# Kernel tuning notes

Measured on AMD Instinct MI355X. Metric: run time of the kernel, lower is better.

## Reference

```python
import jax, jax.numpy as jnp
import numpy as np

N_GRAPHS = 1000
P = 300                 # nodes per ring graph
N = N_GRAPHS * P        # 300000 nodes
IN_DIM = 2
HID = 128
OUT_DIM = 2


def _ring_edges():
    idx = jnp.arange(N)
    g = idx // P
    pos = idx % P
    nxt = g * P + (pos + 1) % P
    src = jnp.concatenate([idx, nxt])
    dst = jnp.concatenate([nxt, idx])
    return jnp.stack([src, dst]), g


def setup_inputs() -> dict:
    key = jax.random.key(0)
    ks = jax.random.split(key, 11)
    edge_index, batch = _ring_edges()
    x = jax.random.normal(ks[0], (N, IN_DIM), jnp.float32)

    def glorot(k, fan_in, fan_out):
        lim = np.sqrt(6.0 / (fan_in + fan_out)).astype(np.float32)
        return jax.random.uniform(k, (fan_in, fan_out), jnp.float32, -lim, lim)

    return {
        "x": x,
        "edge_index": edge_index,
        "batch": batch,
        "W1": glorot(ks[1], IN_DIM, HID), "b1": jnp.zeros((HID,), jnp.float32),
        "W2": glorot(ks[2], HID, HID),    "b2": jnp.zeros((HID,), jnp.float32),
        "W3": glorot(ks[3], HID, HID),    "b3": jnp.zeros((HID,), jnp.float32),
        "fw1": glorot(ks[4], HID, HID),   "fb1": jnp.zeros((HID,), jnp.float32),
        "fw2": glorot(ks[5], HID, OUT_DIM), "fb2": jnp.zeros((OUT_DIM,), jnp.float32),
    }


def _gcn_conv(x, W, b, src, dst, norm):
    h = x @ W                              # [N, out]
    msg = h[src] * norm[:, None]           # gather + per-edge scale
    agg = jax.ops.segment_sum(msg, dst, num_segments=N)  # scatter-add
    return agg + b


def reference(x, edge_index, batch, W1, b1, W2, b2, W3, b3, fw1, fb1, fw2, fb2):
    loop = jnp.arange(N)
    src = jnp.concatenate([edge_index[0], loop])
    dst = jnp.concatenate([edge_index[1], loop])
    deg = jax.ops.segment_sum(jnp.ones_like(dst, jnp.float32), dst, num_segments=N)
    dis = jax.lax.rsqrt(deg)               # deg >= 1 due to self-loops
    norm = dis[src] * dis[dst]             # per-edge normalization

    h = jax.nn.relu(_gcn_conv(x, W1, b1, src, dst, norm))
    h = jax.nn.relu(_gcn_conv(h, W2, b2, src, dst, norm))
    h = jax.nn.relu(_gcn_conv(h, W3, b3, src, dst, norm))

    # global mean pool per graph
    sums = jax.ops.segment_sum(h, batch, num_segments=N_GRAPHS)
    cnts = jax.ops.segment_sum(jnp.ones((N,), jnp.float32), batch, num_segments=N_GRAPHS)
    pooled = sums / cnts[:, None]

    out = jax.nn.relu(pooled @ fw1 + fb1)
    out = out @ fw2 + fb2
    return out
```

## Files before the change

### kernel.cpp

```cpp
#include <hip/hip_runtime.h>
#include <hip/hip_bf16.h>
#include <stdint.h>

#define P    300
#define HID  128
#define NG   1000
#define NTL  19

typedef __attribute__((ext_vector_type(8))) short bf16x8;
typedef __attribute__((ext_vector_type(4))) short bf16x4;
typedef __attribute__((ext_vector_type(4))) float f32x4;

__device__ short g_wsw[2 * HID * HID];

__device__ __forceinline__ short f2bf(float f) {
    union { float f; uint32_t u; } v; v.f = f;
    uint32_t r = v.u + 0x7fffu + ((v.u >> 16) & 1u);
    return (short)(r >> 16);
}
__device__ __forceinline__ uint32_t pkbf2(float a, float b) {
    union { __hip_bfloat162 h; uint32_t u; } cv;
    cv.h = __float22bfloat162_rn(float2{a, b});
    return cv.u;
}

__device__ __forceinline__ f32x4 mfma16(bf16x4 a, bf16x4 b, f32x4 c) {
#if __has_builtin(__builtin_amdgcn_mfma_f32_16x16x16bf16_1k)
    return __builtin_amdgcn_mfma_f32_16x16x16bf16_1k(a, b, c, 0, 0, 0);
#else
    asm("v_mfma_f32_16x16x16_bf16 %0, %1, %2, %0" : "+v"(c) : "v"(a), "v"(b));
    return c;
#endif
}

__global__ __launch_bounds__(256) void k_prep(const float* __restrict__ W2,
                                              const float* __restrict__ W3) {
    int b = blockIdx.x;
    const bool perm = (b < 8);
    const float* W = perm ? W2 : W3;
    short* dst = g_wsw + (perm ? 0 : HID * HID);
    int t    = (b & 7) * 256 + threadIdx.x;
    int fkey = t >> 4;
    int kc   = t & 15;
    int fsrc;
    if (perm) {
        int u = fkey >> 5, ft = (fkey >> 4) & 1, l = fkey & 15;
        fsrc = u * 32 + 2 * l + ft;
    } else fsrc = fkey;
    bf16x8 o;
    #pragma unroll
    for (int j = 0; j < 8; ++j)
        o[j] = f2bf(W[(kc * 8 + j) * HID + fsrc]);
    *(bf16x8*)&dst[(fkey * 16 + (kc ^ (fkey & 15))) * 8] = o;
}

template<int POOL>
__device__ __forceinline__ void run_pass(short* __restrict__ buf,
                                         const short* __restrict__ wbase,
                                         const float* __restrict__ bias,
                                         float* __restrict__ pool, int tid) {
    const int lane = tid & 63, wv = tid >> 6, q = lane >> 4, lm = lane & 15;
    const int ftg0 = wv * 2;
    bf16x8 wf[2][4];
    #pragma unroll
    for (int ft = 0; ft < 2; ++ft) {
        int fkey = (ftg0 + ft) * 16 + lm;
        #pragma unroll
        for (int kk = 0; kk < 4; ++kk)
            wf[ft][kk] = *(const bf16x8*)&wbase[(fkey * 16 + ((4 * kk + q) ^ lm)) * 8];
    }
    float biaf[2];
    #pragma unroll
    for (int ft = 0; ft < 2; ++ft)
        biaf[ft] = POOL ? bias[(ftg0 + ft) * 16 + lm] : bias[wv * 32 + 2 * lm + ft];
    const int fpair = wv * 32 + 2 * lm;
    const int kcs = fpair >> 3, offs = fpair & 7;

    const short ONE = (short)0x3F80;
    bf16x4 Sb = {0, 0, 0, 0}, Sp = {0, 0, 0, 0}, Sn = {0, 0, 0, 0},
           Swa = {0, 0, 0, 0}, Swb = {0, 0, 0, 0};
    #pragma unroll
    for (int j = 0; j < 4; ++j) {
        const int k = 4 * q + j;
        if (((lm & 3) == 0 && k == lm - 1) || ((lm & 3) == 3 && k == lm + 1))
            Sb[j] = ONE;
        if (lm == 0  && k == 15) Sp[j]  = ONE;
        if (lm == 15 && k == 0 ) Sn[j]  = ONE;
        if (lm == 11 && k == 0 ) Swa[j] = ONE;
        if (lm == 0  && k == 11) Swb[j] = ONE;
    }

    float psum[2] = {0.f, 0.f};

    auto mfma_tile = [&](int t, f32x4 (&G)[2]) {
        const short* tb = buf + t * 2048;
        G[0] = f32x4{0.f, 0.f, 0.f, 0.f};
        G[1] = f32x4{0.f, 0.f, 0.f, 0.f};
        #pragma unroll
        for (int kk = 0; kk < 4; ++kk) {
            bf16x8 af = *(const bf16x8*)&tb[(lm * 16 + ((4 * kk + q) ^ lm)) * 8];
            G[0] = __builtin_amdgcn_mfma_f32_16x16x32_bf16(af, wf[0][kk], G[0], 0, 0, 0);
            G[1] = __builtin_amdgcn_mfma_f32_16x16x32_bf16(af, wf[1][kk], G[1], 0, 0, 0);
        }
    };
    auto pack = [&](const f32x4 (&G)[2], bf16x4 (&d)[2]) {
        #pragma unroll
        for (int ft = 0; ft < 2; ++ft) {
            union { bf16x4 v; uint32_t u[2]; } pk;
            pk.u[0] = pkbf2(G[ft][0], G[ft][1]);
            pk.u[1] = pkbf2(G[ft][2], G[ft][3]);
            d[ft] = pk.v;
        }
    };
    auto store_rows = [&](int T, float (&o)[2][4]) {
        #pragma unroll
        for (int i = 0; i < 4; ++i) {
            int node = T * 16 + q * 4 + i;
            *(uint32_t*)&buf[(node * 16 + (kcs ^ (node & 15))) * 8 + offs] =
                pkbf2(o[0][i], o[1][i]);
        }
    };
    auto accum = [&](float (&o)[2][4]) {
        #pragma unroll
        for (int ft = 0; ft < 2; ++ft)
            psum[ft] += o[ft][0] + o[ft][1] + o[ft][2] + o[ft][3];
    };

    auto epi = [&](const f32x4 (&E)[2], const bf16x4 (&bT)[2],
                   const bf16x4 (&bP)[2], const bf16x4 (&bN)[2],
                   int wrap, const bf16x4 (&bW)[2], float (&o)[2][4]) {
        #pragma unroll
        for (int ft = 0; ft < 2; ++ft) {
            f32x4 C = {0.f, 0.f, 0.f, 0.f};
            C = mfma16(Sb, bT[ft], C);
            C = mfma16(Sp, bP[ft], C);
            C = mfma16(Sn, bN[ft], C);
            if (wrap == 1) C = mfma16(Swa, bW[ft], C);
            if (wrap == 2) C = mfma16(Swb, bW[ft], C);
            const float s0 = E[ft][0] + E[ft][1];
            const float s2 = E[ft][2] + E[ft][3];
            float t0 = C[0] + s0;
            float t1 = s0 + E[ft][2];
            float t2 = E[ft][1] + s2;
            float t3 = s2 + C[3];
            float v0 = fmaf(t0, 1.f / 3.f, biaf[ft]);
            float v1 = fmaf(t1, 1.f / 3.f, biaf[ft]);
            float v2 = fmaf(t2, 1.f / 3.f, biaf[ft]);
            float v3 = fmaf(t3, 1.f / 3.f, biaf[ft]);
            o[ft][0] = v0 > 0.f ? v0 : 0.f;
            o[ft][1] = v1 > 0.f ? v1 : 0.f;
            o[ft][2] = v2 > 0.f ? v2 : 0.f;
            o[ft][3] = v3 > 0.f ? v3 : 0.f;
        }
    };

    f32x4 G0c[2], Gp[2], Ga[2], Gb[2];
    bf16x4 bq0[2], bq1[2], bqA[2], bqB[2], bqC[2], bqD[2];

    mfma_tile(0, G0c);
    pack(G0c, bq0);
    bqB[0] = bq0[0]; bqB[1] = bq0[1];
    bqA[0] = bq0[0]; bqA[1] = bq0[1];
    Gp[0] = G0c[0]; Gp[1] = G0c[1];

    for (int j = 1; j <= 9; ++j) {
        mfma_tile(2 * j - 1, Ga); pack(Ga, bqC);
        mfma_tile(2 * j,     Gb); pack(Gb, bqD);
        if (j == 1) { bq1[0] = bqC[0]; bq1[1] = bqC[1]; }
        if (!POOL) __syncthreads();
        if (j > 1) {
            float o[2][4];
            epi(Gp, bqB, bqA, bqC, 0, bq0, o);
            if (POOL) accum(o); else store_rows(2 * j - 2, o);
        }
        {
            float o[2][4];
            epi(Ga, bqC, bqB, bqD, 0, bq0, o);
            if (POOL) accum(o); else store_rows(2 * j - 1, o);
        }
        Gp[0] = Gb[0]; Gp[1] = Gb[1];
        bqA[0] = bqC[0]; bqA[1] = bqC[1];
        bqB[0] = bqD[0]; bqB[1] = bqD[1];
    }

    {
        float o18[2][4];
        epi(Gp, bqB, bqA, bq0, 1, bq0, o18);
        if (q < 3) { if (POOL) accum(o18); else store_rows(18, o18); }
        float o0[2][4];
        epi(G0c, bq0, bqB, bq1, 2, bqB, o0);
        if (POOL) accum(o0); else store_rows(0, o0);
    }

    if (POOL) {
        #pragma unroll
        for (int ft = 0; ft < 2; ++ft) {
            psum[ft] += __shfl_xor(psum[ft], 16, 64);
            psum[ft] += __shfl_xor(psum[ft], 32, 64);
        }
        if (q == 0) {
            pool[ftg0 * 16 + lm]      = psum[0];
            pool[ftg0 * 16 + 16 + lm] = psum[1];
        }
    }
}

__global__ __launch_bounds__(256, 1) void k_graph(
        const float* __restrict__ x,
        const float* __restrict__ W1,  const float* __restrict__ b1,
        const float* __restrict__ b2v, const float* __restrict__ b3v,
        const float* __restrict__ fw1, const float* __restrict__ fb1,
        const float* __restrict__ fw2, const float* __restrict__ fb2,
        float* __restrict__ out) {
    __shared__ __align__(16) short buf[304 * HID];
    __shared__ __align__(16) float scr[640];
    float* xs    = scr;
    float* pool  = scr;
    float* parts = scr + 128;
    float* s1    = scr + 384;

    const int g = blockIdx.x, tid = threadIdx.x;

    if (tid < 150) *(float4*)&xs[tid * 4] = *(const float4*)&x[g * 600 + tid * 4];
    __syncthreads();

    {
        const int kc1 = tid & 15;
        const int n0  = tid >> 4;
        float w1x[8], w1y[8], b1v[8];
        #pragma unroll
        for (int j = 0; j < 8; ++j) {
            w1x[j] = W1[kc1 * 8 + j];
            w1y[j] = W1[HID + kc1 * 8 + j];
            b1v[j] = b1[kc1 * 8 + j];
        }
        #pragma unroll
        for (int it = 0; it < NTL; ++it) {
            int node = it * 16 + n0;
            uint32_t w[4] = {0u, 0u, 0u, 0u};
            if (node < P) {
                int prev = (node == 0)     ? P - 1 : node - 1;
                int next = (node == P - 1) ? 0     : node + 1;
                float2 xp = *(const float2*)&xs[2 * prev];
                float2 xc = *(const float2*)&xs[2 * node];
                float2 xn = *(const float2*)&xs[2 * next];
                float ax = (xp.x + xc.x + xn.x) * (1.f / 3.f);
                float ay = (xp.y + xc.y + xn.y) * (1.f / 3.f);
                #pragma unroll
                for (int jj = 0; jj < 4; ++jj) {
                    float va = ax * w1x[2*jj]   + ay * w1y[2*jj]   + b1v[2*jj];
                    float vb = ax * w1x[2*jj+1] + ay * w1y[2*jj+1] + b1v[2*jj+1];
                    va = va > 0.f ? va : 0.f;
                    vb = vb > 0.f ? vb : 0.f;
                    w[jj] = pkbf2(va, vb);
                }
            }
            *(uint4*)&buf[(node * 16 + (kc1 ^ (node & 15))) * 8] =
                uint4{w[0], w[1], w[2], w[3]};
        }
    }
    __syncthreads();

    run_pass<0>(buf, g_wsw,             b2v, pool, tid);
    __syncthreads();
    run_pass<1>(buf, g_wsw + HID * HID, b3v, pool, tid);
    __syncthreads();

    {
        int f = tid & 127, half = tid >> 7;
        float p = 0.f;
        const float* fw1c = fw1 + f;
        #pragma unroll 4
        for (int k = half * 64; k < half * 64 + 64; ++k)
            p += pool[k] * fw1c[k * 128];
        parts[half * 128 + f] = p;
    }
    __syncthreads();
    if (tid < 128) {
        float o1 = fb1[tid] + (parts[tid] + parts[128 + tid]) * (1.0f / 300.0f);
        s1[tid] = o1 > 0.f ? o1 : 0.f;
    }
    __syncthreads();
    if (tid < 128) {
        int o = tid >> 6, ln = tid & 63;
        float v = s1[ln] * fw2[ln * 2 + o] + s1[ln + 64] * fw2[(ln + 64) * 2 + o];
        #pragma unroll
        for (int off = 1; off <= 32; off <<= 1)
            v += __shfl_xor(v, off, 64);
        if (ln == 0) out[g * 2 + o] = v + fb2[o];
    }
}

extern "C" void kernel_launch(void* const* d_in, const int* in_sizes, int n_in,
                              void* d_out, int out_size, void* d_ws, size_t ws_size,
                              hipStream_t stream) {
    const float* x   = (const float*)d_in[0];
    const float* W1  = (const float*)d_in[3];
    const float* b1  = (const float*)d_in[4];
    const float* W2  = (const float*)d_in[5];
    const float* b2  = (const float*)d_in[6];
    const float* W3  = (const float*)d_in[7];
    const float* b3  = (const float*)d_in[8];
    const float* fw1 = (const float*)d_in[9];
    const float* fb1 = (const float*)d_in[10];
    const float* fw2 = (const float*)d_in[11];
    const float* fb2 = (const float*)d_in[12];
    float* out = (float*)d_out;

    k_prep <<<dim3(16), dim3(256), 0, stream>>>(W2, W3);
    k_graph<<<dim3(NG), dim3(256), 0, stream>>>(x, W1, b1, b2, b3,
                                                fw1, fb1, fw2, fb2, out);
}
```

Measured before the change: 130.1 us.

## Double block size so each wave owns one 16-feature tile

```diff
diff --git a/kernel.cpp b/kernel.cpp
--- a/kernel.cpp
+++ b/kernel.cpp
@@ -36,21 +36,15 @@
 __global__ __launch_bounds__(256) void k_prep(const float* __restrict__ W2,
                                               const float* __restrict__ W3) {
     int b = blockIdx.x;
-    const bool perm = (b < 8);
-    const float* W = perm ? W2 : W3;
-    short* dst = g_wsw + (perm ? 0 : HID * HID);
+    const float* W = (b < 8) ? W2 : W3;
+    short* dst = g_wsw + ((b < 8) ? 0 : HID * HID);
     int t    = (b & 7) * 256 + threadIdx.x;
     int fkey = t >> 4;
     int kc   = t & 15;
-    int fsrc;
-    if (perm) {
-        int u = fkey >> 5, ft = (fkey >> 4) & 1, l = fkey & 15;
-        fsrc = u * 32 + 2 * l + ft;
-    } else fsrc = fkey;
     bf16x8 o;
     #pragma unroll
     for (int j = 0; j < 8; ++j)
-        o[j] = f2bf(W[(kc * 8 + j) * HID + fsrc]);
+        o[j] = f2bf(W[(kc * 8 + j) * HID + fkey]);
     *(bf16x8*)&dst[(fkey * 16 + (kc ^ (fkey & 15))) * 8] = o;
 }
 
@@ -60,21 +54,13 @@
                                          const float* __restrict__ bias,
                                          float* __restrict__ pool, int tid) {
     const int lane = tid & 63, wv = tid >> 6, q = lane >> 4, lm = lane & 15;
-    const int ftg0 = wv * 2;
-    bf16x8 wf[2][4];
+    const int fkey = wv * 16 + lm;
+    bf16x8 wf[4];
     #pragma unroll
-    for (int ft = 0; ft < 2; ++ft) {
-        int fkey = (ftg0 + ft) * 16 + lm;
-        #pragma unroll
-        for (int kk = 0; kk < 4; ++kk)
-            wf[ft][kk] = *(const bf16x8*)&wbase[(fkey * 16 + ((4 * kk + q) ^ lm)) * 8];
-    }
-    float biaf[2];
-    #pragma unroll
-    for (int ft = 0; ft < 2; ++ft)
-        biaf[ft] = POOL ? bias[(ftg0 + ft) * 16 + lm] : bias[wv * 32 + 2 * lm + ft];
-    const int fpair = wv * 32 + 2 * lm;
-    const int kcs = fpair >> 3, offs = fpair & 7;
+    for (int kk = 0; kk < 4; ++kk)
+        wf[kk] = *(const bf16x8*)&wbase[(fkey * 16 + ((4 * kk + q) ^ lm)) * 8];
+    const float biaf = bias[fkey];
+    const int kcs = fkey >> 3, offs = fkey & 7;
 
     const short ONE = (short)0x3F80;
     bf16x4 Sb = {0, 0, 0, 0}, Sp = {0, 0, 0, 0}, Sn = {0, 0, 0, 0},
@@ -90,122 +76,101 @@
         if (lm == 0  && k == 11) Swb[j] = ONE;
     }
 
-    float psum[2] = {0.f, 0.f};
-
-    auto mfma_tile = [&](int t, f32x4 (&G)[2]) {
+    float psum = 0.f;
+
+    auto mfma_tile = [&](int t, f32x4 &G) {
         const short* tb = buf + t * 2048;
-        G[0] = f32x4{0.f, 0.f, 0.f, 0.f};
-        G[1] = f32x4{0.f, 0.f, 0.f, 0.f};
+        G = f32x4{0.f, 0.f, 0.f, 0.f};
         #pragma unroll
         for (int kk = 0; kk < 4; ++kk) {
             bf16x8 af = *(const bf16x8*)&tb[(lm * 16 + ((4 * kk + q) ^ lm)) * 8];
-            G[0] = __builtin_amdgcn_mfma_f32_16x16x32_bf16(af, wf[0][kk], G[0], 0, 0, 0);
-            G[1] = __builtin_amdgcn_mfma_f32_16x16x32_bf16(af, wf[1][kk], G[1], 0, 0, 0);
-        }
-    };
-    auto pack = [&](const f32x4 (&G)[2], bf16x4 (&d)[2]) {
-        #pragma unroll
-        for (int ft = 0; ft < 2; ++ft) {
-            union { bf16x4 v; uint32_t u[2]; } pk;
-            pk.u[0] = pkbf2(G[ft][0], G[ft][1]);
-            pk.u[1] = pkbf2(G[ft][2], G[ft][3]);
-            d[ft] = pk.v;
-        }
-    };
-    auto store_rows = [&](int T, float (&o)[2][4]) {
+            G = __builtin_amdgcn_mfma_f32_16x16x32_bf16(af, wf[kk], G, 0, 0, 0);
+        }
+    };
+    auto pack = [&](const f32x4 &G, bf16x4 &d) {
+        union { bf16x4 v; uint32_t u[2]; } pk;
+        pk.u[0] = pkbf2(G[0], G[1]);
+        pk.u[1] = pkbf2(G[2], G[3]);
+        d = pk.v;
+    };
+    auto store_rows = [&](int T, float (&o)[4]) {
         #pragma unroll
         for (int i = 0; i < 4; ++i) {
             int node = T * 16 + q * 4 + i;
-            *(uint32_t*)&buf[(node * 16 + (kcs ^ (node & 15))) * 8 + offs] =
-                pkbf2(o[0][i], o[1][i]);
-        }
-    };
-    auto accum = [&](float (&o)[2][4]) {
-        #pragma unroll
-        for (int ft = 0; ft < 2; ++ft)
-            psum[ft] += o[ft][0] + o[ft][1] + o[ft][2] + o[ft][3];
-    };
-
-    auto epi = [&](const f32x4 (&E)[2], const bf16x4 (&bT)[2],
-                   const bf16x4 (&bP)[2], const bf16x4 (&bN)[2],
-                   int wrap, const bf16x4 (&bW)[2], float (&o)[2][4]) {
-        #pragma unroll
-        for (int ft = 0; ft < 2; ++ft) {
-            f32x4 C = {0.f, 0.f, 0.f, 0.f};
-            C = mfma16(Sb, bT[ft], C);
-            C = mfma16(Sp, bP[ft], C);
-            C = mfma16(Sn, bN[ft], C);
-            if (wrap == 1) C = mfma16(Swa, bW[ft], C);
-            if (wrap == 2) C = mfma16(Swb, bW[ft], C);
-            const float s0 = E[ft][0] + E[ft][1];
-            const float s2 = E[ft][2] + E[ft][3];
-            float t0 = C[0] + s0;
-            float t1 = s0 + E[ft][2];
-            float t2 = E[ft][1] + s2;
-            float t3 = s2 + C[3];
-            float v0 = fmaf(t0, 1.f / 3.f, biaf[ft]);
-            float v1 = fmaf(t1, 1.f / 3.f, biaf[ft]);
-            float v2 = fmaf(t2, 1.f / 3.f, biaf[ft]);
-            float v3 = fmaf(t3, 1.f / 3.f, biaf[ft]);
-            o[ft][0] = v0 > 0.f ? v0 : 0.f;
-            o[ft][1] = v1 > 0.f ? v1 : 0.f;
-            o[ft][2] = v2 > 0.f ? v2 : 0.f;
-            o[ft][3] = v3 > 0.f ? v3 : 0.f;
-        }
-    };
-
-    f32x4 G0c[2], Gp[2], Ga[2], Gb[2];
-    bf16x4 bq0[2], bq1[2], bqA[2], bqB[2], bqC[2], bqD[2];
+            buf[(node * 16 + (kcs ^ (node & 15))) * 8 + offs] = f2bf(o[i]);
+        }
+    };
+    auto accum = [&](float (&o)[4]) { psum += o[0] + o[1] + o[2] + o[3]; };
+
+    auto epi = [&](const f32x4 &E, const bf16x4 &bT, const bf16x4 &bP,
+                   const bf16x4 &bN, int wrap, const bf16x4 &bW,
+                   float (&o)[4]) {
+        f32x4 C = {0.f, 0.f, 0.f, 0.f};
+        C = mfma16(Sb, bT, C);
+        C = mfma16(Sp, bP, C);
+        C = mfma16(Sn, bN, C);
+        if (wrap == 1) C = mfma16(Swa, bW, C);
+        if (wrap == 2) C = mfma16(Swb, bW, C);
+        const float s0 = E[0] + E[1];
+        const float s2 = E[2] + E[3];
+        float t0 = C[0] + s0;
+        float t1 = s0 + E[2];
+        float t2 = E[1] + s2;
+        float t3 = s2 + C[3];
+        float v0 = fmaf(t0, 1.f / 3.f, biaf);
+        float v1 = fmaf(t1, 1.f / 3.f, biaf);
+        float v2 = fmaf(t2, 1.f / 3.f, biaf);
+        float v3 = fmaf(t3, 1.f / 3.f, biaf);
+        o[0] = v0 > 0.f ? v0 : 0.f;
+        o[1] = v1 > 0.f ? v1 : 0.f;
+        o[2] = v2 > 0.f ? v2 : 0.f;
+        o[3] = v3 > 0.f ? v3 : 0.f;
+    };
+
+    f32x4 G0c, Gp, Ga, Gb;
+    bf16x4 bq0, bq1, bqA, bqB, bqC, bqD;
 
     mfma_tile(0, G0c);
     pack(G0c, bq0);
-    bqB[0] = bq0[0]; bqB[1] = bq0[1];
-    bqA[0] = bq0[0]; bqA[1] = bq0[1];
-    Gp[0] = G0c[0]; Gp[1] = G0c[1];
+    bqB = bq0;
+    bqA = bq0;
+    Gp = G0c;
 
     for (int j = 1; j <= 9; ++j) {
         mfma_tile(2 * j - 1, Ga); pack(Ga, bqC);
         mfma_tile(2 * j,     Gb); pack(Gb, bqD);
-        if (j == 1) { bq1[0] = bqC[0]; bq1[1] = bqC[1]; }
+        if (j == 1) bq1 = bqC;
         if (!POOL) __syncthreads();
         if (j > 1) {
-            float o[2][4];
+            float o[4];
             epi(Gp, bqB, bqA, bqC, 0, bq0, o);
             if (POOL) accum(o); else store_rows(2 * j - 2, o);
         }
         {
-            float o[2][4];
+            float o[4];
             epi(Ga, bqC, bqB, bqD, 0, bq0, o);
             if (POOL) accum(o); else store_rows(2 * j - 1, o);
         }
-        Gp[0] = Gb[0]; Gp[1] = Gb[1];
-        bqA[0] = bqC[0]; bqA[1] = bqC[1];
-        bqB[0] = bqD[0]; bqB[1] = bqD[1];
+        Gp = Gb; bqA = bqC; bqB = bqD;
     }
 
     {
-        float o18[2][4];
+        float o18[4];
         epi(Gp, bqB, bqA, bq0, 1, bq0, o18);
         if (q < 3) { if (POOL) accum(o18); else store_rows(18, o18); }
-        float o0[2][4];
+        float o0[4];
         epi(G0c, bq0, bqB, bq1, 2, bqB, o0);
         if (POOL) accum(o0); else store_rows(0, o0);
     }
 
     if (POOL) {
-        #pragma unroll
-        for (int ft = 0; ft < 2; ++ft) {
-            psum[ft] += __shfl_xor(psum[ft], 16, 64);
-            psum[ft] += __shfl_xor(psum[ft], 32, 64);
-        }
-        if (q == 0) {
-            pool[ftg0 * 16 + lm]      = psum[0];
-            pool[ftg0 * 16 + 16 + lm] = psum[1];
-        }
-    }
-}
-
-__global__ __launch_bounds__(256, 1) void k_graph(
+        psum += __shfl_xor(psum, 16, 64);
+        psum += __shfl_xor(psum, 32, 64);
+        if (q == 0) pool[fkey] = psum;
+    }
+}
+
+__global__ __launch_bounds__(512, 1) void k_graph(
         const float* __restrict__ x,
         const float* __restrict__ W1,  const float* __restrict__ b1,
         const float* __restrict__ b2v, const float* __restrict__ b3v,
@@ -235,28 +200,30 @@
             b1v[j] = b1[kc1 * 8 + j];
         }
         #pragma unroll
-        for (int it = 0; it < NTL; ++it) {
-            int node = it * 16 + n0;
-            uint32_t w[4] = {0u, 0u, 0u, 0u};
-            if (node < P) {
-                int prev = (node == 0)     ? P - 1 : node - 1;
-                int next = (node == P - 1) ? 0     : node + 1;
-                float2 xp = *(const float2*)&xs[2 * prev];
-                float2 xc = *(const float2*)&xs[2 * node];
-                float2 xn = *(const float2*)&xs[2 * next];
-                float ax = (xp.x + xc.x + xn.x) * (1.f / 3.f);
-                float ay = (xp.y + xc.y + xn.y) * (1.f / 3.f);
-                #pragma unroll
-                for (int jj = 0; jj < 4; ++jj) {
-                    float va = ax * w1x[2*jj]   + ay * w1y[2*jj]   + b1v[2*jj];
-                    float vb = ax * w1x[2*jj+1] + ay * w1y[2*jj+1] + b1v[2*jj+1];
-                    va = va > 0.f ? va : 0.f;
-                    vb = vb > 0.f ? vb : 0.f;
-                    w[jj] = pkbf2(va, vb);
+        for (int it = 0; it < 10; ++it) {
+            int node = it * 32 + n0;
+            if (node < 304) {
+                uint32_t w[4] = {0u, 0u, 0u, 0u};
+                if (node < P) {
+                    int prev = (node == 0)     ? P - 1 : node - 1;
+                    int next = (node == P - 1) ? 0     : node + 1;
+                    float2 xp = *(const float2*)&xs[2 * prev];
+                    float2 xc = *(const float2*)&xs[2 * node];
+                    float2 xn = *(const float2*)&xs[2 * next];
+                    float ax = (xp.x + xc.x + xn.x) * (1.f / 3.f);
+                    float ay = (xp.y + xc.y + xn.y) * (1.f / 3.f);
+                    #pragma unroll
+                    for (int jj = 0; jj < 4; ++jj) {
+                        float va = ax * w1x[2*jj]   + ay * w1y[2*jj]   + b1v[2*jj];
+                        float vb = ax * w1x[2*jj+1] + ay * w1y[2*jj+1] + b1v[2*jj+1];
+                        va = va > 0.f ? va : 0.f;
+                        vb = vb > 0.f ? vb : 0.f;
+                        w[jj] = pkbf2(va, vb);
+                    }
                 }
+                *(uint4*)&buf[(node * 16 + (kc1 ^ (node & 15))) * 8] =
+                    uint4{w[0], w[1], w[2], w[3]};
             }
-            *(uint4*)&buf[(node * 16 + (kc1 ^ (node & 15))) * 8] =
-                uint4{w[0], w[1], w[2], w[3]};
         }
     }
     __syncthreads();
@@ -266,7 +233,7 @@
     run_pass<1>(buf, g_wsw + HID * HID, b3v, pool, tid);
     __syncthreads();
 
-    {
+    if (tid < 256) {
         int f = tid & 127, half = tid >> 7;
         float p = 0.f;
         const float* fw1c = fw1 + f;
@@ -308,6 +275,6 @@
     float* out = (float*)d_out;
 
     k_prep <<<dim3(16), dim3(256), 0, stream>>>(W2, W3);
-    k_graph<<<dim3(NG), dim3(256), 0, stream>>>(x, W1, b1, b2, b3,
+    k_graph<<<dim3(NG), dim3(512), 0, stream>>>(x, W1, b1, b2, b3,
                                                 fw1, fb1, fw2, fb2, out);
 }
```

Result: faster. 125.8 us (-3.3%).

## Split each graph's ring across two wave groups with 512-thread blocks

Applied to the files above, without the earlier changes.

```diff
diff --git a/kernel.cpp b/kernel.cpp
--- a/kernel.cpp
+++ b/kernel.cpp
@@ -18,10 +18,17 @@
     uint32_t r = v.u + 0x7fffu + ((v.u >> 16) & 1u);
     return (short)(r >> 16);
 }
+__device__ __forceinline__ float bf2f(short s) {
+    union { uint32_t u; float f; } v; v.u = ((uint32_t)(uint16_t)s) << 16;
+    return v.f;
+}
 __device__ __forceinline__ uint32_t pkbf2(float a, float b) {
     union { __hip_bfloat162 h; uint32_t u; } cv;
     cv.h = __float22bfloat162_rn(float2{a, b});
     return cv.u;
+}
+__device__ __forceinline__ float unpk(int v, int ft) {
+    return bf2f((short)(ft ? (((uint32_t)v) >> 16) : (v & 0xffff)));
 }
 
 __device__ __forceinline__ f32x4 mfma16(bf16x4 a, bf16x4 b, f32x4 c) {
@@ -59,8 +66,10 @@
                                          const short* __restrict__ wbase,
                                          const float* __restrict__ bias,
                                          float* __restrict__ pool, int tid) {
-    const int lane = tid & 63, wv = tid >> 6, q = lane >> 4, lm = lane & 15;
-    const int ftg0 = wv * 2;
+    const int lane = tid & 63, wv = tid >> 6;
+    const int grp = wv >> 2, w4 = wv & 3;
+    const int q = lane >> 4, lm = lane & 15;
+    const int ftg0 = w4 * 2;
     bf16x8 wf[2][4];
     #pragma unroll
     for (int ft = 0; ft < 2; ++ft) {
@@ -72,25 +81,23 @@
     float biaf[2];
     #pragma unroll
     for (int ft = 0; ft < 2; ++ft)
-        biaf[ft] = POOL ? bias[(ftg0 + ft) * 16 + lm] : bias[wv * 32 + 2 * lm + ft];
-    const int fpair = wv * 32 + 2 * lm;
+        biaf[ft] = POOL ? bias[(ftg0 + ft) * 16 + lm] : bias[w4 * 32 + 2 * lm + ft];
+    const int fpair = w4 * 32 + 2 * lm;
     const int kcs = fpair >> 3, offs = fpair & 7;
 
     const short ONE = (short)0x3F80;
-    bf16x4 Sb = {0, 0, 0, 0}, Sp = {0, 0, 0, 0}, Sn = {0, 0, 0, 0},
-           Swa = {0, 0, 0, 0}, Swb = {0, 0, 0, 0};
+    bf16x4 Sb = {0, 0, 0, 0}, Sp = {0, 0, 0, 0}, Sn = {0, 0, 0, 0};
     #pragma unroll
     for (int j = 0; j < 4; ++j) {
         const int k = 4 * q + j;
         if (((lm & 3) == 0 && k == lm - 1) || ((lm & 3) == 3 && k == lm + 1))
             Sb[j] = ONE;
-        if (lm == 0  && k == 15) Sp[j]  = ONE;
-        if (lm == 15 && k == 0 ) Sn[j]  = ONE;
-        if (lm == 11 && k == 0 ) Swa[j] = ONE;
-        if (lm == 0  && k == 11) Swb[j] = ONE;
+        if (lm == 0  && k == 15) Sp[j] = ONE;
+        if (lm == 15 && k == 0 ) Sn[j] = ONE;
     }
 
     float psum[2] = {0.f, 0.f};
+    float z[2];
 
     auto mfma_tile = [&](int t, f32x4 (&G)[2]) {
         const short* tb = buf + t * 2048;
@@ -128,21 +135,21 @@
 
     auto epi = [&](const f32x4 (&E)[2], const bf16x4 (&bT)[2],
                    const bf16x4 (&bP)[2], const bf16x4 (&bN)[2],
-                   int wrap, const bf16x4 (&bW)[2], float (&o)[2][4]) {
+                   int mode, float (&o)[2][4]) {
         #pragma unroll
         for (int ft = 0; ft < 2; ++ft) {
             f32x4 C = {0.f, 0.f, 0.f, 0.f};
             C = mfma16(Sb, bT[ft], C);
-            C = mfma16(Sp, bP[ft], C);
-            C = mfma16(Sn, bN[ft], C);
-            if (wrap == 1) C = mfma16(Swa, bW[ft], C);
-            if (wrap == 2) C = mfma16(Swb, bW[ft], C);
+            if (mode != 1) C = mfma16(Sp, bP[ft], C);
+            if (mode != 2) C = mfma16(Sn, bN[ft], C);
             const float s0 = E[ft][0] + E[ft][1];
             const float s2 = E[ft][2] + E[ft][3];
             float t0 = C[0] + s0;
             float t1 = s0 + E[ft][2];
             float t2 = E[ft][1] + s2;
             float t3 = s2 + C[3];
+            if (mode == 1) t0 += (q == 0) ? z[ft] : 0.f;
+            if (mode == 2) t3 += (q == 2) ? z[ft] : 0.f;
             float v0 = fmaf(t0, 1.f / 3.f, biaf[ft]);
             float v1 = fmaf(t1, 1.f / 3.f, biaf[ft]);
             float v2 = fmaf(t2, 1.f / 3.f, biaf[ft]);
@@ -154,42 +161,73 @@
         }
     };
 
-    f32x4 G0c[2], Gp[2], Ga[2], Gb[2];
-    bf16x4 bq0[2], bq1[2], bqA[2], bqB[2], bqC[2], bqD[2];
-
-    mfma_tile(0, G0c);
-    pack(G0c, bq0);
-    bqB[0] = bq0[0]; bqB[1] = bq0[1];
-    bqA[0] = bq0[0]; bqA[1] = bq0[1];
-    Gp[0] = G0c[0]; Gp[1] = G0c[1];
-
-    for (int j = 1; j <= 9; ++j) {
-        mfma_tile(2 * j - 1, Ga); pack(Ga, bqC);
-        mfma_tile(2 * j,     Gb); pack(Gb, bqD);
-        if (j == 1) { bq1[0] = bqC[0]; bq1[1] = bqC[1]; }
+    const int base = grp ? 10 : 0;
+    f32x4 Gh[2];
+    bf16x4 bqM[2], bqH[2], bq9p[2];
+
+    {
+        f32x4 T[2];
+        if (grp == 0) {
+            mfma_tile(18, T);
+            int v = __shfl((int)pkbf2(T[0][3], T[1][3]), 32 + lm, 64);
+            z[0] = unpk(v, 0); z[1] = unpk(v, 1);
+            mfma_tile(9, T); pack(T, bq9p);
+            Gh[0] = T[0]; Gh[1] = T[1];
+            bqM[0] = bq9p[0]; bqM[1] = bq9p[1];
+            bqH[0] = bq9p[0]; bqH[1] = bq9p[1];
+        } else {
+            mfma_tile(0, T);
+            int v = __shfl((int)pkbf2(T[0][0], T[1][0]), lm, 64);
+            z[0] = unpk(v, 0); z[1] = unpk(v, 1);
+            mfma_tile(8, T); pack(T, bqM);
+            mfma_tile(9, Gh); pack(Gh, bqH);
+            bq9p[0] = bqM[0]; bq9p[1] = bqM[1];
+        }
+    }
+
+    for (int j = 1; j <= 5; ++j) {
+        f32x4 Gc[2], Gd[2];
+        bf16x4 bqC[2], bqD[2];
+        if (j < 5) {
+            int t0r = base + 2 * j - 2;
+            mfma_tile(t0r,     Gc); pack(Gc, bqC);
+            mfma_tile(t0r + 1, Gd); pack(Gd, bqD);
+        } else {
+            mfma_tile(base + 8, Gc); pack(Gc, bqC);
+        }
         if (!POOL) __syncthreads();
-        if (j > 1) {
+
+        if (j == 1 && grp == 0) {
             float o[2][4];
-            epi(Gp, bqB, bqA, bqC, 0, bq0, o);
-            if (POOL) accum(o); else store_rows(2 * j - 2, o);
-        }
-        {
+            epi(Gc, bqC, bqC, bqD, 1, o);
+            if (POOL) accum(o); else store_rows(0, o);
+        } else if (j < 5) {
+            int Ta = base + 2 * j - 3;
             float o[2][4];
-            epi(Ga, bqC, bqB, bqD, 0, bq0, o);
-            if (POOL) accum(o); else store_rows(2 * j - 1, o);
-        }
-        Gp[0] = Gb[0]; Gp[1] = Gb[1];
-        bqA[0] = bqC[0]; bqA[1] = bqC[1];
-        bqB[0] = bqD[0]; bqB[1] = bqD[1];
-    }
-
-    {
-        float o18[2][4];
-        epi(Gp, bqB, bqA, bq0, 1, bq0, o18);
-        if (q < 3) { if (POOL) accum(o18); else store_rows(18, o18); }
-        float o0[2][4];
-        epi(G0c, bq0, bqB, bq1, 2, bqB, o0);
-        if (POOL) accum(o0); else store_rows(0, o0);
+            epi(Gh, bqH, bqM, bqC, 0, o);
+            if (POOL) accum(o); else store_rows(Ta, o);
+            float o2[2][4];
+            epi(Gc, bqC, bqH, bqD, 0, o2);
+            if (POOL) accum(o2); else store_rows(Ta + 1, o2);
+        } else {
+            float o[2][4];
+            epi(Gh, bqH, bqM, bqC, 0, o);
+            if (POOL) accum(o); else store_rows(base + 7, o);
+            if (grp == 0) {
+                float o2[2][4];
+                epi(Gc, bqC, bqH, bq9p, 0, o2);
+                if (POOL) accum(o2); else store_rows(8, o2);
+            } else {
+                float o2[2][4];
+                epi(Gc, bqC, bqH, bqC, 2, o2);
+                if (q < 3) { if (POOL) accum(o2); else store_rows(18, o2); }
+            }
+        }
+        if (j < 5) {
+            Gh[0] = Gd[0]; Gh[1] = Gd[1];
+            bqM[0] = bqC[0]; bqM[1] = bqC[1];
+            bqH[0] = bqD[0]; bqH[1] = bqD[1];
+        }
     }
 
     if (POOL) {
@@ -199,13 +237,13 @@
             psum[ft] += __shfl_xor(psum[ft], 32, 64);
         }
         if (q == 0) {
-            pool[ftg0 * 16 + lm]      = psum[0];
-            pool[ftg0 * 16 + 16 + lm] = psum[1];
-        }
-    }
-}
-
-__global__ __launch_bounds__(256, 1) void k_graph(
+            pool[grp * 128 + ftg0 * 16 + lm]      = psum[0];
+            pool[grp * 128 + ftg0 * 16 + 16 + lm] = psum[1];
+        }
+    }
+}
+
+__global__ __launch_bounds__(512, 2) void k_graph(
         const float* __restrict__ x,
         const float* __restrict__ W1,  const float* __restrict__ b1,
         const float* __restrict__ b2v, const float* __restrict__ b3v,
@@ -215,9 +253,9 @@
     __shared__ __align__(16) short buf[304 * HID];
     __shared__ __align__(16) float scr[640];
     float* xs    = scr;
-    float* pool  = scr;
-    float* parts = scr + 128;
-    float* s1    = scr + 384;
+    float* poolv = scr;
+    float* parts = scr + 256;
+    float* s1    = scr + 512;
 
     const int g = blockIdx.x, tid = threadIdx.x;
 
@@ -235,44 +273,46 @@
             b1v[j] = b1[kc1 * 8 + j];
         }
         #pragma unroll
-        for (int it = 0; it < NTL; ++it) {
-            int node = it * 16 + n0;
-            uint32_t w[4] = {0u, 0u, 0u, 0u};
-            if (node < P) {
-                int prev = (node == 0)     ? P - 1 : node - 1;
-                int next = (node == P - 1) ? 0     : node + 1;
-                float2 xp = *(const float2*)&xs[2 * prev];
-                float2 xc = *(const float2*)&xs[2 * node];
-                float2 xn = *(const float2*)&xs[2 * next];
-                float ax = (xp.x + xc.x + xn.x) * (1.f / 3.f);
-                float ay = (xp.y + xc.y + xn.y) * (1.f / 3.f);
-                #pragma unroll
-                for (int jj = 0; jj < 4; ++jj) {
-                    float va = ax * w1x[2*jj]   + ay * w1y[2*jj]   + b1v[2*jj];
-                    float vb = ax * w1x[2*jj+1] + ay * w1y[2*jj+1] + b1v[2*jj+1];
-                    va = va > 0.f ? va : 0.f;
-                    vb = vb > 0.f ? vb : 0.f;
-                    w[jj] = pkbf2(va, vb);
+        for (int it = 0; it < 10; ++it) {
+            int node = it * 32 + n0;
+            if (node < 304) {
+                uint32_t w[4] = {0u, 0u, 0u, 0u};
+                if (node < P) {
+                    int prev = (node == 0)     ? P - 1 : node - 1;
+                    int next = (node == P - 1) ? 0     : node + 1;
+                    float2 xp = *(const float2*)&xs[2 * prev];
+                    float2 xc = *(const float2*)&xs[2 * node];
+                    float2 xn = *(const float2*)&xs[2 * next];
+                    float ax = (xp.x + xc.x + xn.x) * (1.f / 3.f);
+                    float ay = (xp.y + xc.y + xn.y) * (1.f / 3.f);
+                    #pragma unroll
+                    for (int jj = 0; jj < 4; ++jj) {
+                        float va = ax * w1x[2*jj]   + ay * w1y[2*jj]   + b1v[2*jj];
+                        float vb = ax * w1x[2*jj+1] + ay * w1y[2*jj+1] + b1v[2*jj+1];
+                        va = va > 0.f ? va : 0.f;
+                        vb = vb > 0.f ? vb : 0.f;
+                        w[jj] = pkbf2(va, vb);
+                    }
                 }
+                *(uint4*)&buf[(node * 16 + (kc1 ^ (node & 15))) * 8] =
+                    uint4{w[0], w[1], w[2], w[3]};
             }
-            *(uint4*)&buf[(node * 16 + (kc1 ^ (node & 15))) * 8] =
-                uint4{w[0], w[1], w[2], w[3]};
-        }
-    }
-    __syncthreads();
-
-    run_pass<0>(buf, g_wsw,             b2v, pool, tid);
-    __syncthreads();
-    run_pass<1>(buf, g_wsw + HID * HID, b3v, pool, tid);
-    __syncthreads();
-
-    {
+        }
+    }
+    __syncthreads();
+
+    run_pass<0>(buf, g_wsw,             b2v, poolv, tid);
+    __syncthreads();
+    run_pass<1>(buf, g_wsw + HID * HID, b3v, poolv, tid);
+    __syncthreads();
+
+    if (tid < 256) {
         int f = tid & 127, half = tid >> 7;
         float p = 0.f;
         const float* fw1c = fw1 + f;
         #pragma unroll 4
         for (int k = half * 64; k < half * 64 + 64; ++k)
-            p += pool[k] * fw1c[k * 128];
+            p += (poolv[k] + poolv[128 + k]) * fw1c[k * 128];
         parts[half * 128 + f] = p;
     }
     __syncthreads();
@@ -308,6 +348,6 @@
     float* out = (float*)d_out;
 
     k_prep <<<dim3(16), dim3(256), 0, stream>>>(W2, W3);
-    k_graph<<<dim3(NG), dim3(256), 0, stream>>>(x, W1, b1, b2, b3,
+    k_graph<<<dim3(NG), dim3(512), 0, stream>>>(x, W1, b1, b2, b3,
                                                 fw1, fb1, fw2, fb2, out);
 }
```

Result: slower. 146.7 us (+12.8%).
